# Kernel optimization log

Hardware: AMD Instinct MI355X
Metric: run time of the kernel (lower is better)

## Reference

```python
import jax, jax.numpy as jnp
import numpy as np

WAY = 5
SHOT = 5
SCALE = 10.0
EPS = 1e-8


def setup_inputs() -> dict:
    key = jax.random.key(0)
    k1, k2 = jax.random.split(key, 2)
    x = jax.random.normal(k1, (100, 512, 16, 16), dtype=jnp.float32)
    W = jax.random.normal(k2, (512, 512), dtype=jnp.float32) * 0.02  # 1x1 conv weight (outC, inC)
    b = jnp.zeros((512,), dtype=jnp.float32)
    return {"x": x, "W": W, "b": b}


def reference(x, W, b):
    B, C, H, Wd = x.shape
    # extract(): 1x1 conv -> softmax over flattened (C*H*W) per sample -> remask
    mask = jnp.einsum('bchw,oc->bohw', x, W) + b[None, :, None, None]
    mask = jax.nn.softmax(mask.reshape(B, -1), axis=1).reshape(B, C, H, Wd)
    x = x * mask
    # predict(): (way, shot+query, C, H, W)
    xv = x.reshape(WAY, -1, C, H, Wd)
    s = xv[:, :SHOT].mean(axis=(1, 3, 4))                    # (m=way, d=C) support prototypes
    q = xv[:, SHOT:].reshape(-1, C, H * Wd)                  # (n, d=C, f=H*W) queries
    # cosine_similarity over d, without materializing (n,m,d,f)
    qn = jnp.maximum(jnp.sqrt(jnp.sum(q * q, axis=1)), EPS)  # (n, f)
    sn = jnp.maximum(jnp.sqrt(jnp.sum(s * s, axis=1)), EPS)  # (m,)
    scores = jnp.einsum('ndf,md->nmf', q, s) / (qn[:, None, :] * sn[None, :, None])
    # softmax over classes (m), then mean over spatial positions f
    return jax.nn.softmax(SCALE * scores, axis=1).mean(axis=2)  # (n, way)
```

## Files before the change

### kernel.cpp

```cpp
#include <hip/hip_runtime.h>
#include <hip/hip_bf16.h>
#include <math.h>

typedef _Float16 half8 __attribute__((ext_vector_type(8)));
typedef float f32x4 __attribute__((ext_vector_type(4)));

#define BATCH 100
#define CH    512
#define HWP   256
#define SAMP  (CH * HWP)

__device__ __forceinline__ void async16(const void* g, void* l) {
  __builtin_amdgcn_global_load_lds(
      (const __attribute__((address_space(1))) unsigned int*)g,
      (__attribute__((address_space(3))) unsigned int*)l, 16, 0, 0);
}

__global__ __launch_bounds__(256) void k_txpose(const float* __restrict__ x,
                                               _Float16* __restrict__ xh,
                                               const float* __restrict__ W,
                                               _Float16* __restrict__ Wh,
                                               float* __restrict__ denom) {
  __shared__ float tb[64][69];
  int bid  = blockIdx.x;
  if (bid >= 3200) {
    int base = (bid - 3200) * 1024 + threadIdx.x;
#pragma unroll
    for (int j = 0; j < 4; j++) Wh[base + j * 256] = (_Float16)W[base + j * 256];
    if (bid == 3200 && threadIdx.x < 128) denom[threadIdx.x] = 0.0f;
    return;
  }
  int b    = bid >> 5;
  int tile = bid & 31;
  int c0 = (tile >> 2) << 6;
  int p0 = (tile & 3) << 6;
  int t = threadIdx.x;
  const float* xb = x + (size_t)b * SAMP;
#pragma unroll
  for (int it = 0; it < 4; it++) {
    int ch = it * 256 + t;
    int c  = ch >> 4;
    int pc = (ch & 15) << 2;
    float4 v = *(const float4*)(xb + (size_t)(c0 + c) * HWP + p0 + pc);
    tb[c][pc] = v.x; tb[c][pc + 1] = v.y; tb[c][pc + 2] = v.z; tb[c][pc + 3] = v.w;
  }
  __syncthreads();
  _Float16* xhb = xh + (size_t)b * SAMP;
#pragma unroll
  for (int it = 0; it < 2; it++) {
    int ch = it * 256 + t;
    int p  = ch >> 3;
    int ck = (ch & 7) << 3;
    half8 h;
#pragma unroll
    for (int j = 0; j < 8; j++) h[j] = (_Float16)tb[ck + j][p];
    *(half8*)(xhb + (size_t)(p0 + p) * CH + c0 + ck) = h;
  }
}

__global__ __launch_bounds__(256) void k_gemm(const _Float16* __restrict__ Wh,
                                             const _Float16* __restrict__ xh,
                                             const float* __restrict__ bias,
                                             _Float16* __restrict__ u,
                                             float* __restrict__ denom) {
  __shared__ __align__(16) _Float16 smem[128 * 136];
  int bid = blockIdx.x;
  int w     = (bid & 7) * 100 + (bid >> 3);
  int batch = w >> 3;
  int sub   = w & 7;
  int ot = sub & 3, pt = sub >> 2;
  int o0 = ot * 128, p0 = pt * 128;
  const _Float16* Bg = xh + (size_t)batch * SAMP;

  int t  = threadIdx.x;
  int wv = t >> 6, ln = t & 63;
  int qd = ln >> 4, r = ln & 15;
  int wm0 = (wv >> 1) * 64, wn0 = (wv & 1) * 64;

  auto stage = [&](int q, int kk) {
    _Float16* As = smem + q * 8192;
    _Float16* Bs = As + 4096;
#pragma unroll
    for (int it = 0; it < 2; it++) {
      int ch  = it * 256 + t;
      int row = ch >> 2;
      int qc  = ch & 3;
      char* la = (char*)As + (size_t)(it * 256 + wv * 64) * 16;
      char* lb = (char*)Bs + (size_t)(it * 256 + wv * 64) * 16;
      async16((const char*)(Wh + (size_t)(o0 + row) * 512 + kk + qc * 8), la);
      async16((const char*)(Bg + (size_t)(p0 + row) * 512 + kk + qc * 8), lb);
    }
  };

  f32x4 acc[4][4] = {};
  stage(0, 0);

  for (int ks = 0; ks < 16; ks++) {
    int q = ks & 1;
    if (ks < 15) {
      stage(q ^ 1, (ks + 1) * 32);
      asm volatile("s_waitcnt vmcnt(4)" ::: "memory");
    } else {
      asm volatile("s_waitcnt vmcnt(0)" ::: "memory");
    }
    __builtin_amdgcn_s_barrier();
    asm volatile("" ::: "memory");
    const _Float16* As = smem + q * 8192;
    const _Float16* Bs = As + 4096;
    half8 af[4], bf[4];
#pragma unroll
    for (int i = 0; i < 4; i++)
      af[i] = *(const half8*)(As + (wm0 + i * 16 + r) * 32 + qd * 8);
#pragma unroll
    for (int j = 0; j < 4; j++)
      bf[j] = *(const half8*)(Bs + (wn0 + j * 16 + r) * 32 + qd * 8);
#pragma unroll
    for (int i = 0; i < 4; i++)
#pragma unroll
      for (int j = 0; j < 4; j++)
        acc[i][j] = __builtin_amdgcn_mfma_f32_16x16x32_f16(af[i], bf[j], acc[i][j], 0, 0, 0);
    asm volatile("" ::: "memory");
    __builtin_amdgcn_s_barrier();
  }

#pragma unroll
  for (int it = 0; it < 8; it++) {
    int ch = it * 256 + t;
    int p  = ch >> 4;
    int ck = ch & 15;
    half8 v = *(const half8*)(Bg + (size_t)(p0 + p) * CH + o0 + ck * 8);
    *(half8*)(smem + p * 136 + ck * 8) = v;
  }
  __syncthreads();

  _Float16* outb = u + (size_t)batch * SAMP;
  float lsum = 0.f;
#pragma unroll
  for (int i = 0; i < 4; i++) {
#pragma unroll
    for (int rg = 0; rg < 4; rg++) {
      int ol = wm0 + i * 16 + qd * 4 + rg;
      float bv = bias[o0 + ol];
#pragma unroll
      for (int j = 0; j < 4; j++) {
        int pl = wn0 + j * 16 + r;
        float ev = __expf(acc[i][j][rg] + bv);
        lsum += ev;
        float xv = (float)smem[pl * 136 + ol];
        outb[(size_t)(o0 + ol) * HWP + p0 + pl] = (_Float16)(xv * ev);
      }
    }
  }
#pragma unroll
  for (int off = 32; off; off >>= 1) lsum += __shfl_down(lsum, off, 64);
  __shared__ float rs[4];
  if (ln == 0) rs[wv] = lsum;
  __syncthreads();
  if (t == 0) atomicAdd(&denom[batch], rs[0] + rs[1] + rs[2] + rs[3]);
}

__global__ __launch_bounds__(256) void k_proto(const _Float16* __restrict__ u,
                                              const float* __restrict__ denom,
                                              float* __restrict__ sproto) {
  int c = blockIdx.x;
  int t = threadIdx.x;
  int wv = t >> 6;
  float accm[5];
#pragma unroll
  for (int m = 0; m < 5; m++) {
    float acc = 0.f;
#pragma unroll
    for (int j = 0; j < 5; j++) {
      int b = m * 20 + j;
      acc += (float)u[(size_t)b * SAMP + (size_t)c * HWP + t] * (1.0f / denom[b]);
    }
    accm[m] = acc;
  }
#pragma unroll
  for (int m = 0; m < 5; m++) {
    float v = accm[m];
#pragma unroll
    for (int off = 32; off; off >>= 1) v += __shfl_down(v, off, 64);
    accm[m] = v;
  }
  __shared__ float rs[4][5];
  if ((t & 63) == 0) {
#pragma unroll
    for (int m = 0; m < 5; m++) rs[wv][m] = accm[m];
  }
  __syncthreads();
  if (t < 5) sproto[t * 512 + c] =
      (rs[0][t] + rs[1][t] + rs[2][t] + rs[3][t]) * (1.0f / 1280.0f);
}

__global__ __launch_bounds__(256) void k_part(const _Float16* __restrict__ u,
                                             const float* __restrict__ sproto,
                                             float* __restrict__ part) {
  __shared__ float s_l[5 * 64];
  int n = blockIdx.x >> 3, gc = blockIdx.x & 7;
  int b = (n / 15) * 20 + 5 + (n % 15);
  int t = threadIdx.x;
  for (int i = t; i < 320; i += 256)
    s_l[i] = sproto[(i >> 6) * 512 + gc * 64 + (i & 63)];
  __syncthreads();
  const _Float16* ub = u + (size_t)b * SAMP + (size_t)gc * 64 * HWP;
  float dot[5] = {0, 0, 0, 0, 0}, qq = 0.f;
#pragma unroll 8
  for (int c = 0; c < 64; c++) {
    float v = (float)ub[c * HWP + t];
    qq += v * v;
#pragma unroll
    for (int m = 0; m < 5; m++) dot[m] += v * s_l[m * 64 + c];
  }
  float* pp = part + (size_t)(n * 8 + gc) * 6 * 256 + t;
  pp[0 * 256] = dot[0]; pp[1 * 256] = dot[1]; pp[2 * 256] = dot[2];
  pp[3 * 256] = dot[3]; pp[4 * 256] = dot[4]; pp[5 * 256] = qq;
}

__global__ __launch_bounds__(256) void k_comb(const float* __restrict__ part,
                                             const float* __restrict__ sproto,
                                             float* __restrict__ out) {
  int n = blockIdx.x, t = threadIdx.x;
  int wv = t >> 6;
  __shared__ float prefs[5];
  __shared__ float rsn[4][5];
  {
    float sn2[5];
#pragma unroll
    for (int m = 0; m < 5; m++) {
      float v1 = sproto[m * 512 + t], v2 = sproto[m * 512 + 256 + t];
      sn2[m] = v1 * v1 + v2 * v2;
    }
#pragma unroll
    for (int m = 0; m < 5; m++) {
      float v = sn2[m];
#pragma unroll
      for (int off = 32; off; off >>= 1) v += __shfl_down(v, off, 64);
      sn2[m] = v;
    }
    if ((t & 63) == 0) {
#pragma unroll
      for (int m = 0; m < 5; m++) rsn[wv][m] = sn2[m];
    }
    __syncthreads();
    if (t < 5) prefs[t] =
        10.0f / fmaxf(sqrtf(rsn[0][t] + rsn[1][t] + rsn[2][t] + rsn[3][t]), 1e-8f);
    __syncthreads();
  }
  float dot[5] = {0, 0, 0, 0, 0}, qq = 0.f;
#pragma unroll
  for (int gc = 0; gc < 8; gc++) {
    const float* pp = part + (size_t)(n * 8 + gc) * 6 * 256 + t;
    dot[0] += pp[0 * 256]; dot[1] += pp[1 * 256]; dot[2] += pp[2 * 256];
    dot[3] += pp[3 * 256]; dot[4] += pp[4 * 256]; qq += pp[5 * 256];
  }
  float iqn = 1.0f / fmaxf(sqrtf(qq), 1e-20f);
  float sc[5], mx = -1e30f;
#pragma unroll
  for (int m = 0; m < 5; m++) { sc[m] = dot[m] * prefs[m] * iqn; mx = fmaxf(mx, sc[m]); }
  float p[5], ssum = 0.f;
#pragma unroll
  for (int m = 0; m < 5; m++) { p[m] = __expf(sc[m] - mx); ssum += p[m]; }
  float rr = 1.0f / ssum;
#pragma unroll
  for (int m = 0; m < 5; m++) {
    float v = p[m] * rr;
#pragma unroll
    for (int off = 32; off; off >>= 1) v += __shfl_down(v, off, 64);
    p[m] = v;
  }
  __shared__ float rs[4][5];
  if ((t & 63) == 0) {
#pragma unroll
    for (int m = 0; m < 5; m++) rs[t >> 6][m] = p[m];
  }
  __syncthreads();
  if (t < 5) out[n * 5 + t] =
      (rs[0][t] + rs[1][t] + rs[2][t] + rs[3][t]) * (1.0f / 256.0f);
}

extern "C" void kernel_launch(void* const* d_in, const int* in_sizes, int n_in,
                              void* d_out, int out_size, void* d_ws, size_t ws_size,
                              hipStream_t stream) {
  const float* x    = (const float*)d_in[0];
  const float* W    = (const float*)d_in[1];
  const float* bias = (const float*)d_in[2];
  float* out = (float*)d_out;

  char* ws = (char*)d_ws;
  _Float16* xh     = (_Float16*)(ws + 0);
  float*    part   = (float*)   (ws + 0);
  _Float16* Wh     = (_Float16*)(ws + 26214400);
  _Float16* u      = (_Float16*)(ws + 26738688);
  float*    denom  = (float*)   (ws + 52953088);
  float*    sproto = (float*)   (ws + 52953600);

  k_txpose <<<3456, 256, 0, stream>>>(x, xh, W, Wh, denom);
  k_gemm   <<<800,  256, 0, stream>>>(Wh, xh, bias, u, denom);
  k_proto  <<<512,  256, 0, stream>>>(u, denom, sproto);
  k_part   <<<600,  256, 0, stream>>>(u, sproto, part);
  k_comb   <<<75,   256, 0, stream>>>(part, sproto, out);
}
```

Baseline: 134.7 us.

## Fuse support prototype reduction into GEMM epilogue and drop k_proto kernel

Support-sample GEMM tiles no longer write the masked activations to the fp16 buffer. They reduce each channel's masked sum over spatial positions in registers and atomically add it into a small per-batch raw buffer, which is zeroed in the transpose kernel. The prototype kernel is removed, and k_part and k_comb rebuild the prototypes from the raw sums divided by the softmax denominators. This saves one launch and the support-sample writes and reads of u. In exchange it adds shuffles and atomics in the epilogue, branch divergence between support and query batches, and repeated prototype reconstruction in the downstream kernels.

```diff
diff --git a/kernel.cpp b/kernel.cpp
--- a/kernel.cpp
+++ b/kernel.cpp
@@ -20,7 +20,8 @@
                                                _Float16* __restrict__ xh,
                                                const float* __restrict__ W,
                                                _Float16* __restrict__ Wh,
-                                               float* __restrict__ denom) {
+                                               float* __restrict__ denom,
+                                               float* __restrict__ raw) {
   __shared__ float tb[64][69];
   int bid  = blockIdx.x;
   if (bid >= 3200) {
@@ -28,6 +29,11 @@
 #pragma unroll
     for (int j = 0; j < 4; j++) Wh[base + j * 256] = (_Float16)W[base + j * 256];
     if (bid == 3200 && threadIdx.x < 128) denom[threadIdx.x] = 0.0f;
+    if (bid >= 3201 && bid < 3251) {
+      int rb = (bid - 3201) * 1024 + threadIdx.x;
+#pragma unroll
+      for (int j = 0; j < 4; j++) raw[rb + j * 256] = 0.0f;
+    }
     return;
   }
   int b    = bid >> 5;
@@ -62,7 +68,8 @@
                                              const _Float16* __restrict__ xh,
                                              const float* __restrict__ bias,
                                              _Float16* __restrict__ u,
-                                             float* __restrict__ denom) {
+                                             float* __restrict__ denom,
+                                             float* __restrict__ raw) {
   __shared__ __align__(16) _Float16 smem[128 * 136];
   int bid = blockIdx.x;
   int w     = (bid & 7) * 100 + (bid >> 3);
@@ -133,21 +140,46 @@
   }
   __syncthreads();
 
+  bool is_supp = (batch % 20) < 5;
   _Float16* outb = u + (size_t)batch * SAMP;
   float lsum = 0.f;
-#pragma unroll
-  for (int i = 0; i < 4; i++) {
-#pragma unroll
-    for (int rg = 0; rg < 4; rg++) {
-      int ol = wm0 + i * 16 + qd * 4 + rg;
-      float bv = bias[o0 + ol];
-#pragma unroll
-      for (int j = 0; j < 4; j++) {
-        int pl = wn0 + j * 16 + r;
-        float ev = __expf(acc[i][j][rg] + bv);
-        lsum += ev;
-        float xv = (float)smem[pl * 136 + ol];
-        outb[(size_t)(o0 + ol) * HWP + p0 + pl] = (_Float16)(xv * ev);
+  if (!is_supp) {
+#pragma unroll
+    for (int i = 0; i < 4; i++) {
+#pragma unroll
+      for (int rg = 0; rg < 4; rg++) {
+        int ol = wm0 + i * 16 + qd * 4 + rg;
+        float bv = bias[o0 + ol];
+#pragma unroll
+        for (int j = 0; j < 4; j++) {
+          int pl = wn0 + j * 16 + r;
+          float ev = __expf(acc[i][j][rg] + bv);
+          lsum += ev;
+          float xv = (float)smem[pl * 136 + ol];
+          outb[(size_t)(o0 + ol) * HWP + p0 + pl] = (_Float16)(xv * ev);
+        }
+      }
+    }
+  } else {
+    float* rawb = raw + (size_t)batch * 512 + o0;
+#pragma unroll
+    for (int i = 0; i < 4; i++) {
+#pragma unroll
+      for (int rg = 0; rg < 4; rg++) {
+        int ol = wm0 + i * 16 + qd * 4 + rg;
+        float bv = bias[o0 + ol];
+        float s4 = 0.f;
+#pragma unroll
+        for (int j = 0; j < 4; j++) {
+          int pl = wn0 + j * 16 + r;
+          float ev = __expf(acc[i][j][rg] + bv);
+          lsum += ev;
+          float xv = (float)smem[pl * 136 + ol];
+          s4 += xv * ev;
+        }
+#pragma unroll
+        for (int off = 1; off < 16; off <<= 1) s4 += __shfl_xor(s4, off, 64);
+        if (r == 0) atomicAdd(&rawb[ol], s4);
       }
     }
   }
@@ -159,49 +191,25 @@
   if (t == 0) atomicAdd(&denom[batch], rs[0] + rs[1] + rs[2] + rs[3]);
 }
 
-__global__ __launch_bounds__(256) void k_proto(const _Float16* __restrict__ u,
-                                              const float* __restrict__ denom,
-                                              float* __restrict__ sproto) {
-  int c = blockIdx.x;
-  int t = threadIdx.x;
-  int wv = t >> 6;
-  float accm[5];
-#pragma unroll
-  for (int m = 0; m < 5; m++) {
-    float acc = 0.f;
-#pragma unroll
-    for (int j = 0; j < 5; j++) {
-      int b = m * 20 + j;
-      acc += (float)u[(size_t)b * SAMP + (size_t)c * HWP + t] * (1.0f / denom[b]);
-    }
-    accm[m] = acc;
-  }
-#pragma unroll
-  for (int m = 0; m < 5; m++) {
-    float v = accm[m];
-#pragma unroll
-    for (int off = 32; off; off >>= 1) v += __shfl_down(v, off, 64);
-    accm[m] = v;
-  }
-  __shared__ float rs[4][5];
-  if ((t & 63) == 0) {
-#pragma unroll
-    for (int m = 0; m < 5; m++) rs[wv][m] = accm[m];
-  }
-  __syncthreads();
-  if (t < 5) sproto[t * 512 + c] =
-      (rs[0][t] + rs[1][t] + rs[2][t] + rs[3][t]) * (1.0f / 1280.0f);
-}
-
 __global__ __launch_bounds__(256) void k_part(const _Float16* __restrict__ u,
-                                             const float* __restrict__ sproto,
+                                             const float* __restrict__ raw,
+                                             const float* __restrict__ denom,
                                              float* __restrict__ part) {
   __shared__ float s_l[5 * 64];
   int n = blockIdx.x >> 3, gc = blockIdx.x & 7;
   int b = (n / 15) * 20 + 5 + (n % 15);
   int t = threadIdx.x;
-  for (int i = t; i < 320; i += 256)
-    s_l[i] = sproto[(i >> 6) * 512 + gc * 64 + (i & 63)];
+  for (int i = t; i < 320; i += 256) {
+    int m = i >> 6, cl = i & 63;
+    int c = gc * 64 + cl;
+    float s = 0.f;
+#pragma unroll
+    for (int j = 0; j < 5; j++) {
+      int sb = m * 20 + j;
+      s += raw[sb * 512 + c] / denom[sb];
+    }
+    s_l[i] = s * (1.0f / 1280.0f);
+  }
   __syncthreads();
   const _Float16* ub = u + (size_t)b * SAMP + (size_t)gc * 64 * HWP;
   float dot[5] = {0, 0, 0, 0, 0}, qq = 0.f;
@@ -218,7 +226,8 @@
 }
 
 __global__ __launch_bounds__(256) void k_comb(const float* __restrict__ part,
-                                             const float* __restrict__ sproto,
+                                             const float* __restrict__ raw,
+                                             const float* __restrict__ denom,
                                              float* __restrict__ out) {
   int n = blockIdx.x, t = threadIdx.x;
   int wv = t >> 6;
@@ -228,8 +237,16 @@
     float sn2[5];
 #pragma unroll
     for (int m = 0; m < 5; m++) {
-      float v1 = sproto[m * 512 + t], v2 = sproto[m * 512 + 256 + t];
-      sn2[m] = v1 * v1 + v2 * v2;
+      float s1 = 0.f, s2 = 0.f;
+#pragma unroll
+      for (int j = 0; j < 5; j++) {
+        int sb = m * 20 + j;
+        float inv = 1.0f / denom[sb];
+        s1 += raw[sb * 512 + t] * inv;
+        s2 += raw[sb * 512 + 256 + t] * inv;
+      }
+      s1 *= (1.0f / 1280.0f); s2 *= (1.0f / 1280.0f);
+      sn2[m] = s1 * s1 + s2 * s2;
     }
 #pragma unroll
     for (int m = 0; m < 5; m++) {
@@ -293,11 +310,10 @@
   _Float16* Wh     = (_Float16*)(ws + 26214400);
   _Float16* u      = (_Float16*)(ws + 26738688);
   float*    denom  = (float*)   (ws + 52953088);
-  float*    sproto = (float*)   (ws + 52953600);
-
-  k_txpose <<<3456, 256, 0, stream>>>(x, xh, W, Wh, denom);
-  k_gemm   <<<800,  256, 0, stream>>>(Wh, xh, bias, u, denom);
-  k_proto  <<<512,  256, 0, stream>>>(u, denom, sproto);
-  k_part   <<<600,  256, 0, stream>>>(u, sproto, part);
-  k_comb   <<<75,   256, 0, stream>>>(part, sproto, out);
-}
+  float*    raw    = (float*)   (ws + 52953600);
+
+  k_txpose <<<3456, 256, 0, stream>>>(x, xh, W, Wh, denom, raw);
+  k_gemm   <<<800,  256, 0, stream>>>(Wh, xh, bias, u, denom, raw);
+  k_part   <<<600,  256, 0, stream>>>(u, raw, denom, part);
+  k_comb   <<<75,   256, 0, stream>>>(part, raw, denom, out);
+}
```

New measurement: 134.7 us. No clear change (-0.0%).
